# Kernel tuning notes

Hardware: AMD Instinct MI355X
Metric: run time of the kernel (lower is better)

Reference implementation:

```python
import jax, jax.numpy as jnp
import numpy as np

V, E, T, U, C, B = 50000, 300, 512, 256, 20, 64


def _rn(k, shape):
    return jax.random.normal(k, shape, jnp.float32) * 0.05


def setup_inputs() -> dict:
    key = jax.random.key(0)
    ks = jax.random.split(key, 16)
    G = 3 * U  # gate width (z, r, h)
    return {
        "x": jax.random.randint(ks[0], (B, T), 0, V),
        "emb": _rn(ks[1], (V, E)),
        "k1f": _rn(ks[2], (E, G)), "rk1f": _rn(ks[3], (U, G)), "b1f": jnp.zeros((2, G), jnp.float32),
        "k1b": _rn(ks[4], (E, G)), "rk1b": _rn(ks[5], (U, G)), "b1b": jnp.zeros((2, G), jnp.float32),
        "k2f": _rn(ks[6], (2 * U, G)), "rk2f": _rn(ks[7], (U, G)), "b2f": jnp.zeros((2, G), jnp.float32),
        "k2b": _rn(ks[8], (2 * U, G)), "rk2b": _rn(ks[9], (U, G)), "b2b": jnp.zeros((2, G), jnp.float32),
        "wout": _rn(ks[10], (2 * U, C)), "bout": jnp.zeros((C,), jnp.float32),
    }


def gru_dir(x_seq, k, rk, b, reverse):
    """Keras GRU (reset_after=True), one direction. x_seq: [B,T,D] -> [B,T,U]."""
    # precompute input projections for all timesteps (big GEMM once)
    xw = jnp.einsum('btd,dg->btg', x_seq, k) + b[0]  # [B,T,3U]
    if reverse:
        xw = xw[:, ::-1]
    u = rk.shape[0]

    def step(h, xt):
        inner = h @ rk + b[1]                      # [B,3U]
        xz, xr, xh = jnp.split(xt, 3, axis=-1)
        rz, rr, rh = jnp.split(inner, 3, axis=-1)
        z = jax.nn.sigmoid(xz + rz)
        r = jax.nn.sigmoid(xr + rr)
        hh = jnp.tanh(xh + r * rh)
        hn = z * h + (1.0 - z) * hh
        return hn, hn

    h0 = jnp.zeros((x_seq.shape[0], u), x_seq.dtype)
    _, hs = jax.lax.scan(step, h0, jnp.swapaxes(xw, 0, 1))  # [T,B,U]
    hs = jnp.swapaxes(hs, 0, 1)                             # [B,T,U]
    return hs[:, ::-1] if reverse else hs


def reference(x, emb, k1f, rk1f, b1f, k1b, rk1b, b1b,
              k2f, rk2f, b2f, k2b, rk2b, b2b, wout, bout):
    e = emb[x]                                   # [B,T,E]
    # BiGRU layer 1 (return_sequences=True), concat merge
    f1 = gru_dir(e, k1f, rk1f, b1f, reverse=False)
    b1 = gru_dir(e, k1b, rk1b, b1b, reverse=True)
    h1 = jnp.concatenate([f1, b1], axis=-1)      # [B,T,2U]
    # BiGRU layer 2 (return_sequences=False): last state of each direction
    f2 = gru_dir(h1, k2f, rk2f, b2f, reverse=False)[:, -1]  # [B,U]
    b2 = gru_dir(h1, k2b, rk2b, b2b, reverse=True)[:, 0]    # [B,U]
    h2 = jnp.concatenate([f2, b2], axis=-1)      # [B,2U]
    return jax.nn.softmax(h2 @ wout + bout, axis=-1)  # [B,C]
```

## Files before the change

### kernel.cpp

```cpp
#include <hip/hip_runtime.h>

typedef unsigned char  u8;
typedef unsigned short u16;
typedef unsigned int   u32;
typedef unsigned long long u64;
typedef __attribute__((ext_vector_type(8))) short s8v;
typedef __attribute__((ext_vector_type(4))) float f4v;
typedef __attribute__((ext_vector_type(4))) int   i4v;
typedef __attribute__((ext_vector_type(8))) int   i8v;
typedef __attribute__((ext_vector_type(2))) unsigned int u32x2;

#define B_SZ  64
#define T_LEN 512
#define U_DIM 256
#define E_DIM 300
#define EP    320
#define G3    768
#define NTOT  1536
#define C_DIM 20
#define BT    (B_SZ*T_LEN)

__device__ __forceinline__ float bf2f(u16 h){ return __uint_as_float(((u32)h)<<16); }
__device__ __forceinline__ u16 f2bf(float f){
  u32 u = __float_as_uint(f);
  u32 r = (u + 0x7FFFu + ((u>>16)&1u)) >> 16;
  return (u16)r;
}

__device__ __forceinline__ u8 f2fp8(float f){
  u32 u = __float_as_uint(f);
  u32 s = (u>>24)&0x80u;
  u32 au = u & 0x7fffffffu;
  if(au < 0x3C800000u){
    float m = rintf(__uint_as_float(au) * 512.f);
    return (u8)(s | (u32)(int)m);
  }
  int e = (int)(au>>23) - 127;
  u32 mant = au & 0x7fffffu;
  u32 lsb = (mant>>20)&1u;
  mant += 0x7FFFFu + lsb;
  if(mant >> 23){ mant = 0; e += 1; }
  if(e > 8 || (e==8 && ((mant>>20)&7u)==7u)) return (u8)(s | 0x7Eu);
  return (u8)(s | ((u32)(e+7)<<3) | ((mant>>20)&7u));
}

__global__ void embed_pad(const int* __restrict__ x, const float* __restrict__ emb,
                          u16* __restrict__ e){
  int idx = blockIdx.x*256 + threadIdx.x;
  if(idx >= BT*EP) return;
  int row = idx / EP, col = idx - row*EP;
  u16 v = 0;
  if(col < E_DIM) v = f2bf(emb[(size_t)x[row]*E_DIM + col]);
  e[idx] = v;
}

__global__ void transpose_cc(const float* __restrict__ A, const float* __restrict__ Bm,
                             u16* __restrict__ dst, int K, int Kp, int N){
  int idx = blockIdx.x*256 + threadIdx.x;
  if(idx >= N*Kp) return;
  int n = idx / Kp, k = idx - n*Kp;
  u16 v = 0;
  if(k < K){
    const float* s = (n < G3) ? A : Bm;
    int nn = (n < G3) ? n : n - G3;
    v = f2bf(s[(size_t)k*G3 + nn]);
  }
  dst[idx] = v;
}

__global__ void transpose_fp8(const float* __restrict__ rk, u8* __restrict__ dst){
  int idx = blockIdx.x*256 + threadIdx.x;
  if(idx >= G3*U_DIM) return;
  int n = idx >> 8, k = idx & 255;
  dst[idx] = f2fp8(rk[(size_t)k*G3 + n]);
}

__global__ __launch_bounds__(256) void gemm_bt(
    const u16* __restrict__ A, const u16* __restrict__ BT_, u16* __restrict__ Cq,
    int Kp, const float* __restrict__ biasA, const float* __restrict__ biasB)
{
  __shared__ u16 Al[128][40];
  __shared__ u16 Bl[128][40];
  int tid = threadIdx.x;
  int w = tid>>6, l = tid&63, lc = l&15, quad = l>>4;
  int wm = w>>1, wn = w&1;
  int nb = blockIdx.x*128;
  int bg4 = blockIdx.y >> 4, tg = blockIdx.y & 15;
  int b0r = bg4*4, tb0 = tg*32;

  f4v acc[4][4];
  #pragma unroll
  for(int i=0;i<4;i++)
    #pragma unroll
    for(int j=0;j<4;j++) acc[i][j] = (f4v){0.f,0.f,0.f,0.f};

  int nk = Kp >> 5;
  for(int kt=0; kt<nk; kt++){
    __syncthreads();
    {
      int c0 = tid, c1 = tid + 256;
      int r0 = c0>>2, k80 = c0&3;
      int r1 = c1>>2, k81 = c1&3;
      size_t ga0 = ((size_t)(b0r + (r0&3))*T_LEN + tb0 + (r0>>2))*Kp;
      size_t ga1 = ((size_t)(b0r + (r1&3))*T_LEN + tb0 + (r1>>2))*Kp;
      *(s8v*)&Al[r0][k80*8] = *(const s8v*)(A + ga0 + kt*32 + k80*8);
      *(s8v*)&Al[r1][k81*8] = *(const s8v*)(A + ga1 + kt*32 + k81*8);
      *(s8v*)&Bl[r0][k80*8] = *(const s8v*)(BT_ + (size_t)(nb+r0)*Kp + kt*32 + k80*8);
      *(s8v*)&Bl[r1][k81*8] = *(const s8v*)(BT_ + (size_t)(nb+r1)*Kp + kt*32 + k81*8);
    }
    __syncthreads();
    s8v af[4], bf[4];
    #pragma unroll
    for(int i=0;i<4;i++) af[i] = *(const s8v*)&Al[wm*64 + i*16 + lc][quad*8];
    #pragma unroll
    for(int j=0;j<4;j++) bf[j] = *(const s8v*)&Bl[wn*64 + j*16 + lc][quad*8];
    #pragma unroll
    for(int i=0;i<4;i++)
      #pragma unroll
      for(int j=0;j<4;j++)
        acc[i][j] = __builtin_amdgcn_mfma_f32_16x16x32_bf16(af[i], bf[j], acc[i][j],0,0,0);
  }

  int dirq = (nb >= G3) ? 1 : 0;
  int c7b  = nb - dirq*G3 + wn*64;
  int g    = c7b >> 8;
  int ut0  = (c7b >> 4) & 15;
  const float* bb = dirq ? biasB : biasA;
  float bj[4];
  #pragma unroll
  for(int j=0;j<4;j++){
    int cc = c7b + j*16 + lc;
    bj[j] = bb[cc] + ((g < 2) ? bb[G3 + cc] : 0.f);
  }
  #pragma unroll
  for(int i=0;i<4;i++){
    int t = tb0 + wm*16 + i*4 + quad;
    size_t base = ((((size_t)dirq*T_LEN + t)*B_SZ + b0r)*3 + g)*256 + lc*16 + ut0;
    #pragma unroll
    for(int r=0;r<4;r++){
      u16 p0 = f2bf(acc[i][0][r] + bj[0]);
      u16 p1 = f2bf(acc[i][1][r] + bj[1]);
      u16 p2 = f2bf(acc[i][2][r] + bj[2]);
      u16 p3 = f2bf(acc[i][3][r] + bj[3]);
      *(u64*)(Cq + base + (size_t)r*768) =
        (u64)p0 | ((u64)p1<<16) | ((u64)p2<<32) | ((u64)p3<<48);
    }
  }
}


#define ACLB \
 "a0","a1","a2","a3","a4","a5","a6","a7","a8","a9","a10","a11","a12","a13","a14","a15", \
 "a16","a17","a18","a19","a20","a21","a22","a23","a24","a25","a26","a27","a28","a29","a30","a31", \
 "a32","a33","a34","a35","a36","a37","a38","a39","a40","a41","a42","a43","a44","a45","a46","a47", \
 "a48","a49","a50","a51","a52","a53","a54","a55","a56","a57","a58","a59","a60","a61","a62","a63", \
 "a64","a65","a66","a67","a68","a69","a70","a71","a72","a73","a74","a75","a76","a77","a78","a79", \
 "a80","a81","a82","a83","a84","a85","a86","a87","a88","a89","a90","a91","a92","a93","a94","a95", \
 "a96","a97","a98","a99","a100","a101","a102","a103","a104","a105","a106","a107","a108","a109","a110","a111", \
 "a112","a113","a114","a115","a116","a117","a118","a119","a120","a121","a122","a123","a124","a125","a126","a127", \
 "a128","a129","a130","a131","a132","a133","a134","a135","a136","a137","a138","a139","a140","a141","a142","a143", \
 "a144","a145","a146","a147","a148","a149","a150","a151","a152","a153","a154","a155","a156","a157","a158","a159", \
 "a160","a161","a162","a163","a164","a165","a166","a167","a168","a169","a170","a171","a172","a173","a174","a175", \
 "a176","a177","a178","a179","a180","a181","a182","a183","a184","a185","a186","a187","a188","a189","a190","a191"

#define AFENCE asm volatile("" ::: ACLB)

#define BINIT8(G,S,KT,A0,A1,A2,A3,A4,A5,A6,A7) { \
  const u8* p = rkd + ((size_t)((G)*256 + w*64 + (S)*16 + lc)<<8) + (KT)*128 + quad*32; \
  i4v t0 = *(const i4v*)p; \
  i4v t1 = *(const i4v*)(p+16); \
  asm volatile("v_accvgpr_write_b32 a" #A0 ", %0\n\t" \
               "v_accvgpr_write_b32 a" #A1 ", %1\n\t" \
               "v_accvgpr_write_b32 a" #A2 ", %2\n\t" \
               "v_accvgpr_write_b32 a" #A3 ", %3\n\t" \
               "v_accvgpr_write_b32 a" #A4 ", %4\n\t" \
               "v_accvgpr_write_b32 a" #A5 ", %5\n\t" \
               "v_accvgpr_write_b32 a" #A6 ", %6\n\t" \
               "v_accvgpr_write_b32 a" #A7 ", %7" \
               :: "v"(t0[0]),"v"(t0[1]),"v"(t0[2]),"v"(t0[3]), \
                  "v"(t1[0]),"v"(t1[1]),"v"(t1[2]),"v"(t1[3]) : ACLB); }

#define MFZ8(ACC,AF,AR) \
  asm("v_mfma_f32_16x16x128_f8f6f4 %0, %1, " AR ", 0" : "=&v"(ACC) : "v"(AF))
#define MFA8(ACC,AF,AR) \
  asm("v_mfma_f32_16x16x128_f8f6f4 %0, %1, " AR ", %0" : "+v"(ACC) : "v"(AF))

#define FENCE12 asm volatile("s_nop 7\n\ts_nop 7" \
  : "+v"(acc[0]),"+v"(acc[1]),"+v"(acc[2]),"+v"(acc[3]), \
    "+v"(acc[4]),"+v"(acc[5]),"+v"(acc[6]),"+v"(acc[7]), \
    "+v"(acc[8]),"+v"(acc[9]),"+v"(acc[10]),"+v"(acc[11]) :: ACLB)

#define LBAR asm volatile("s_waitcnt lgkmcnt(0)\n\ts_barrier" ::: ACLB, "memory")

__device__ __forceinline__ float bsel(u32x2 v, int i){
  u32 wv = (i & 2) ? (u32)v[1] : (u32)v[0];
  return __uint_as_float((i & 1) ? (wv & 0xffff0000u) : (wv << 16));
}

#define GATE(UT) { \
  float xz = bsel(cz, UT); \
  float xr = bsel(cr, UT); \
  float xh = bsel(ch, UT); \
  float zf = acc[UT][0]   + xz; \
  float rf = acc[4+UT][0] + xr; \
  float rh = acc[8+UT][0] + b1h[UT]; \
  zf = __builtin_amdgcn_rcpf(1.f + __expf(-zf)); \
  rf = __builtin_amdgcn_rcpf(1.f + __expf(-rf)); \
  float hc = xh + rf*rh; \
  float e2 = __expf(2.f*hc); \
  float th = 1.f - 2.f*__builtin_amdgcn_rcpf(e2 + 1.f); \
  float hn = th + zf*(hpc[UT] - th); \
  hpc[UT] = hn; \
  u32 q8; asm("v_cvt_pk_fp8_f32 %0, %1, %2" : "=v"(q8) : "v"(hn), "v"(hn)); \
  hb8[nxt][quad*4][w*64 + (UT)*16 + lc] = (u8)(q8 & 0xffu); \
  if(MODE == 0) \
    hp[(UT)*16] = f2bf(hn); \
  else if(step == T_LEN-1) \
    h2out[(size_t)(b0+quad)*(2*U_DIM) + dir*U_DIM + w*64 + (UT)*16 + lc] = hn; \
}

template<int MODE>
__global__ __launch_bounds__(256,1) void gru_scan3(
    const u16* __restrict__ xq,
    const u8*  __restrict__ rkq,
    const float* __restrict__ bF, const float* __restrict__ bB,
    u16* __restrict__ h1out,
    float* __restrict__ h2out)
{
  int dir = blockIdx.x & 1, bg = blockIdx.x >> 1;
  int b0 = bg*4;
  int tid = threadIdx.x;
  int w = tid>>6, l = tid&63, lc = l&15, quad = l>>4;

  __shared__ u8 hb8[2][16][272];
  for(int i=tid; i<2*16*272; i+=256) ((u8*)hb8)[i] = 0;

  const u8* rkd = rkq + (size_t)dir*G3*U_DIM;

  BINIT8(0,0,0,  0,1,2,3,4,5,6,7)        BINIT8(0,0,1,  8,9,10,11,12,13,14,15)
  BINIT8(0,1,0, 16,17,18,19,20,21,22,23) BINIT8(0,1,1, 24,25,26,27,28,29,30,31)
  BINIT8(0,2,0, 32,33,34,35,36,37,38,39) BINIT8(0,2,1, 40,41,42,43,44,45,46,47)
  BINIT8(0,3,0, 48,49,50,51,52,53,54,55) BINIT8(0,3,1, 56,57,58,59,60,61,62,63)
  BINIT8(1,0,0, 64,65,66,67,68,69,70,71) BINIT8(1,0,1, 72,73,74,75,76,77,78,79)
  BINIT8(1,1,0, 80,81,82,83,84,85,86,87) BINIT8(1,1,1, 88,89,90,91,92,93,94,95)
  BINIT8(1,2,0, 96,97,98,99,100,101,102,103) BINIT8(1,2,1, 104,105,106,107,108,109,110,111)
  BINIT8(1,3,0, 112,113,114,115,116,117,118,119) BINIT8(1,3,1, 120,121,122,123,124,125,126,127)
  BINIT8(2,0,0, 128,129,130,131,132,133,134,135) BINIT8(2,0,1, 136,137,138,139,140,141,142,143)
  BINIT8(2,1,0, 144,145,146,147,148,149,150,151) BINIT8(2,1,1, 152,153,154,155,156,157,158,159)
  BINIT8(2,2,0, 160,161,162,163,164,165,166,167) BINIT8(2,2,1, 168,169,170,171,172,173,174,175)
  BINIT8(2,3,0, 176,177,178,179,180,181,182,183) BINIT8(2,3,1, 184,185,186,187,188,189,190,191)

  float b1h[4];
  const float* bias1 = (dir ? bB : bF) + G3;
  #pragma unroll
  for(int ut=0; ut<4; ut++) b1h[ut] = bias1[2*U_DIM + w*64 + ut*16 + lc];

  int t0 = dir ? (T_LEN-1) : 0;
  long qstride = dir ? -(long)(64*3*256) : (long)(64*3*256);
  const u16* xp = xq + ((((size_t)dir*T_LEN + t0)*B_SZ + (b0+quad))*3)*256 + lc*16 + w*4;
  long hstride = dir ? -(long)(2*U_DIM) : (long)(2*U_DIM);
  u16* hp = (MODE==0)
    ? (h1out + ((size_t)(b0+quad)*T_LEN + t0)*(2*U_DIM) + dir*U_DIM + w*64 + lc)
    : nullptr;

  float hpc[4] = {0.f, 0.f, 0.f, 0.f};

  u32x2 cz = *(const u32x2*)(xp);
  u32x2 cr = *(const u32x2*)(xp + 256);
  u32x2 ch = *(const u32x2*)(xp + 512);

  __syncthreads();

  int cur = 0;
  for(int step=0; step<T_LEN; step++){
    AFENCE;
    int nxt = cur ^ 1;

    i8v af0, af1;
    {
      const u8* p = &hb8[cur][lc][quad*32];
      i4v lo0 = *(const i4v*)p,        hi0 = *(const i4v*)(p+16);
      i4v lo1 = *(const i4v*)(p+128),  hi1 = *(const i4v*)(p+144);
      af0 = __builtin_shufflevector(lo0, hi0, 0,1,2,3,4,5,6,7);
      af1 = __builtin_shufflevector(lo1, hi1, 0,1,2,3,4,5,6,7);
    }

    const u16* xpn = xp + qstride;
    u32x2 czn = *(const u32x2*)(xpn);
    u32x2 crn = *(const u32x2*)(xpn + 256);
    u32x2 chn = *(const u32x2*)(xpn + 512);

    f4v acc[12];
    MFZ8(acc[0], af0,"a[0:7]");     MFZ8(acc[1], af0,"a[16:23]");
    MFZ8(acc[2], af0,"a[32:39]");   MFZ8(acc[3], af0,"a[48:55]");
    MFZ8(acc[4], af0,"a[64:71]");   MFZ8(acc[5], af0,"a[80:87]");
    MFZ8(acc[6], af0,"a[96:103]");  MFZ8(acc[7], af0,"a[112:119]");
    MFZ8(acc[8], af0,"a[128:135]"); MFZ8(acc[9], af0,"a[144:151]");
    MFZ8(acc[10],af0,"a[160:167]"); MFZ8(acc[11],af0,"a[176:183]");
    MFA8(acc[0], af1,"a[8:15]");    MFA8(acc[1], af1,"a[24:31]");
    MFA8(acc[2], af1,"a[40:47]");   MFA8(acc[3], af1,"a[56:63]");
    MFA8(acc[4], af1,"a[72:79]");   MFA8(acc[5], af1,"a[88:95]");
    MFA8(acc[6], af1,"a[104:111]"); MFA8(acc[7], af1,"a[120:127]");
    MFA8(acc[8], af1,"a[136:143]"); MFA8(acc[9], af1,"a[152:159]");
    MFA8(acc[10],af1,"a[168:175]"); MFA8(acc[11],af1,"a[184:191]");
    FENCE12;

    GATE(0)
    GATE(1)
    GATE(2)
    GATE(3)

    cz = czn; cr = crn; ch = chn;
    xp = xpn;
    if(MODE==0) hp += hstride;
    LBAR;
    cur ^= 1;
  }
}

__global__ void out_softmax(const float* __restrict__ h2, const float* __restrict__ wout,
                            const float* __restrict__ bout, float* __restrict__ out)
{
  __shared__ float lg[C_DIM];
  int b = blockIdx.x, l = threadIdx.x;
  float acc[C_DIM];
  #pragma unroll
  for(int c=0;c<C_DIM;c++) acc[c] = 0.f;
  for(int k=l; k<2*U_DIM; k+=64){
    float hv = h2[b*2*U_DIM + k];
    #pragma unroll
    for(int c=0;c<C_DIM;c++) acc[c] += hv * wout[k*C_DIM + c];
  }
  #pragma unroll
  for(int c=0;c<C_DIM;c++){
    float v = acc[c];
    for(int off=32; off; off>>=1) v += __shfl_down(v, off);
    if(l==0) lg[c] = v + bout[c];
  }
  __syncthreads();
  if(l==0){
    float mx = lg[0];
    for(int c=1;c<C_DIM;c++) mx = fmaxf(mx, lg[c]);
    float sum = 0.f, ex[C_DIM];
    for(int c=0;c<C_DIM;c++){ ex[c] = __expf(lg[c]-mx); sum += ex[c]; }
    for(int c=0;c<C_DIM;c++) out[b*C_DIM + c] = ex[c]/sum;
  }
}

extern "C" void kernel_launch(void* const* d_in, const int* in_sizes, int n_in,
                              void* d_out, int out_size, void* d_ws, size_t ws_size,
                              hipStream_t stream)
{
  const int*   x    = (const int*)d_in[0];
  const float* emb  = (const float*)d_in[1];
  const float* k1f  = (const float*)d_in[2];
  const float* rk1f = (const float*)d_in[3];
  const float* b1f  = (const float*)d_in[4];
  const float* k1b  = (const float*)d_in[5];
  const float* rk1b = (const float*)d_in[6];
  const float* b1b  = (const float*)d_in[7];
  const float* k2f  = (const float*)d_in[8];
  const float* rk2f = (const float*)d_in[9];
  const float* b2f  = (const float*)d_in[10];
  const float* k2b  = (const float*)d_in[11];
  const float* rk2b = (const float*)d_in[12];
  const float* b2b  = (const float*)d_in[13];
  const float* wout = (const float*)d_in[14];
  const float* bout = (const float*)d_in[15];

  char* ws = (char*)d_ws;
  u16*  k1t   = (u16*)(ws);
  u16*  k2t   = (u16*)(ws + 983040);
  u8*   rkq   = (u8*)(ws + 2555904);
  float* h2   = (float*)(ws + 4128768);
  u16*  h1    = (u16*)(ws + 4259840);
  u16*  e_pad = (u16*)(ws + 4259840);
  u16*  xq    = (u16*)(ws + 37814272);

  transpose_cc<<<(NTOT*EP +255)/256,256,0,stream>>>(k1f, k1b, k1t, E_DIM, EP, NTOT);
  transpose_cc<<<(NTOT*512+255)/256,256,0,stream>>>(k2f, k2b, k2t, 512, 512, NTOT);
  transpose_fp8<<<768,256,0,stream>>>(rk1f, rkq);
  transpose_fp8<<<768,256,0,stream>>>(rk1b, rkq + 1*G3*U_DIM);
  transpose_fp8<<<768,256,0,stream>>>(rk2f, rkq + 2*G3*U_DIM);
  transpose_fp8<<<768,256,0,stream>>>(rk2b, rkq + 3*G3*U_DIM);

  embed_pad<<<(BT*EP)/256,256,0,stream>>>(x, emb, e_pad);

  gemm_bt<<<dim3(12,256),256,0,stream>>>(e_pad, k1t, xq, EP, b1f, b1b);
  gru_scan3<0><<<32,256,0,stream>>>(xq, rkq, b1f, b1b, h1, nullptr);

  gemm_bt<<<dim3(12,256),256,0,stream>>>(h1, k2t, xq, 512, b2f, b2b);
  gru_scan3<1><<<32,256,0,stream>>>(xq, rkq + 2*G3*U_DIM, b2f, b2b, nullptr, h2);

  out_softmax<<<64,64,0,stream>>>(h2, wout, bout, (float*)d_out);
}
```

Baseline: 1.119 ms.

## Split GRU recurrence across eight waves and interleave MFMA groups with gates

The recurrent scan kernel now launches 512 threads per block instead of 256. Each wave owns 32 hidden units instead of 64, so it keeps half as many recurrent weight tiles in AGPRs and issues 12 MFMAs per step instead of 24. The MFMAs are split into two groups of three gates each, wrapped in s_setprio, so the gate math for the first half-tile can overlap with the second group's MFMAs. The aim is to shorten the serial per-timestep latency chain, at the cost of a barrier across twice as many waves.

Result: slower. 1.237 ms (+10.5%).

```diff
diff --git a/kernel.cpp b/kernel.cpp
--- a/kernel.cpp
+++ b/kernel.cpp
@@ -8,7 +8,6 @@
 typedef __attribute__((ext_vector_type(4))) float f4v;
 typedef __attribute__((ext_vector_type(4))) int   i4v;
 typedef __attribute__((ext_vector_type(8))) int   i8v;
-typedef __attribute__((ext_vector_type(2))) unsigned int u32x2;
 
 #define B_SZ  64
 #define T_LEN 512
@@ -155,18 +154,12 @@
  "a32","a33","a34","a35","a36","a37","a38","a39","a40","a41","a42","a43","a44","a45","a46","a47", \
  "a48","a49","a50","a51","a52","a53","a54","a55","a56","a57","a58","a59","a60","a61","a62","a63", \
  "a64","a65","a66","a67","a68","a69","a70","a71","a72","a73","a74","a75","a76","a77","a78","a79", \
- "a80","a81","a82","a83","a84","a85","a86","a87","a88","a89","a90","a91","a92","a93","a94","a95", \
- "a96","a97","a98","a99","a100","a101","a102","a103","a104","a105","a106","a107","a108","a109","a110","a111", \
- "a112","a113","a114","a115","a116","a117","a118","a119","a120","a121","a122","a123","a124","a125","a126","a127", \
- "a128","a129","a130","a131","a132","a133","a134","a135","a136","a137","a138","a139","a140","a141","a142","a143", \
- "a144","a145","a146","a147","a148","a149","a150","a151","a152","a153","a154","a155","a156","a157","a158","a159", \
- "a160","a161","a162","a163","a164","a165","a166","a167","a168","a169","a170","a171","a172","a173","a174","a175", \
- "a176","a177","a178","a179","a180","a181","a182","a183","a184","a185","a186","a187","a188","a189","a190","a191"
+ "a80","a81","a82","a83","a84","a85","a86","a87","a88","a89","a90","a91","a92","a93","a94","a95"
 
 #define AFENCE asm volatile("" ::: ACLB)
 
 #define BINIT8(G,S,KT,A0,A1,A2,A3,A4,A5,A6,A7) { \
-  const u8* p = rkd + ((size_t)((G)*256 + w*64 + (S)*16 + lc)<<8) + (KT)*128 + quad*32; \
+  const u8* p = rkd + ((size_t)((G)*256 + w*32 + (S)*16 + lc)<<8) + (KT)*128 + quad*32; \
   i4v t0 = *(const i4v*)p; \
   i4v t1 = *(const i4v*)(p+16); \
   asm volatile("v_accvgpr_write_b32 a" #A0 ", %0\n\t" \
@@ -185,25 +178,24 @@
 #define MFA8(ACC,AF,AR) \
   asm("v_mfma_f32_16x16x128_f8f6f4 %0, %1, " AR ", %0" : "+v"(ACC) : "v"(AF))
 
-#define FENCE12 asm volatile("s_nop 7\n\ts_nop 7" \
-  : "+v"(acc[0]),"+v"(acc[1]),"+v"(acc[2]),"+v"(acc[3]), \
-    "+v"(acc[4]),"+v"(acc[5]),"+v"(acc[6]),"+v"(acc[7]), \
-    "+v"(acc[8]),"+v"(acc[9]),"+v"(acc[10]),"+v"(acc[11]) :: ACLB)
+#define FENCEA asm volatile("s_nop 7\n\ts_nop 7" \
+  : "+v"(acc[0]),"+v"(acc[2]),"+v"(acc[4]) :: ACLB)
+#define FENCEB asm volatile("s_nop 7\n\ts_nop 7" \
+  : "+v"(acc[1]),"+v"(acc[3]),"+v"(acc[5]) :: ACLB)
 
 #define LBAR asm volatile("s_waitcnt lgkmcnt(0)\n\ts_barrier" ::: ACLB, "memory")
 
-__device__ __forceinline__ float bsel(u32x2 v, int i){
-  u32 wv = (i & 2) ? (u32)v[1] : (u32)v[0];
-  return __uint_as_float((i & 1) ? (wv & 0xffff0000u) : (wv << 16));
+__device__ __forceinline__ float bsel2(u32 v, int i){
+  return __uint_as_float(i ? (v & 0xffff0000u) : (v << 16));
 }
 
 #define GATE(UT) { \
-  float xz = bsel(cz, UT); \
-  float xr = bsel(cr, UT); \
-  float xh = bsel(ch, UT); \
+  float xz = bsel2(cz, UT); \
+  float xr = bsel2(cr, UT); \
+  float xh = bsel2(ch, UT); \
   float zf = acc[UT][0]   + xz; \
-  float rf = acc[4+UT][0] + xr; \
-  float rh = acc[8+UT][0] + b1h[UT]; \
+  float rf = acc[2+UT][0] + xr; \
+  float rh = acc[4+UT][0] + b1h[UT]; \
   zf = __builtin_amdgcn_rcpf(1.f + __expf(-zf)); \
   rf = __builtin_amdgcn_rcpf(1.f + __expf(-rf)); \
   float hc = xh + rf*rh; \
@@ -212,15 +204,15 @@
   float hn = th + zf*(hpc[UT] - th); \
   hpc[UT] = hn; \
   u32 q8; asm("v_cvt_pk_fp8_f32 %0, %1, %2" : "=v"(q8) : "v"(hn), "v"(hn)); \
-  hb8[nxt][quad*4][w*64 + (UT)*16 + lc] = (u8)(q8 & 0xffu); \
+  hb8[nxt][quad*4][w*32 + (UT)*16 + lc] = (u8)(q8 & 0xffu); \
   if(MODE == 0) \
     hp[(UT)*16] = f2bf(hn); \
   else if(step == T_LEN-1) \
-    h2out[(size_t)(b0+quad)*(2*U_DIM) + dir*U_DIM + w*64 + (UT)*16 + lc] = hn; \
+    h2out[(size_t)(b0+quad)*(2*U_DIM) + dir*U_DIM + w*32 + (UT)*16 + lc] = hn; \
 }
 
 template<int MODE>
-__global__ __launch_bounds__(256,1) void gru_scan3(
+__global__ __launch_bounds__(512,2) void gru_scan3(
     const u16* __restrict__ xq,
     const u8*  __restrict__ rkq,
     const float* __restrict__ bF, const float* __restrict__ bB,
@@ -233,41 +225,35 @@
   int w = tid>>6, l = tid&63, lc = l&15, quad = l>>4;
 
   __shared__ u8 hb8[2][16][272];
-  for(int i=tid; i<2*16*272; i+=256) ((u8*)hb8)[i] = 0;
+  for(int i=tid; i<2*16*272; i+=512) ((u8*)hb8)[i] = 0;
 
   const u8* rkd = rkq + (size_t)dir*G3*U_DIM;
 
   BINIT8(0,0,0,  0,1,2,3,4,5,6,7)        BINIT8(0,0,1,  8,9,10,11,12,13,14,15)
   BINIT8(0,1,0, 16,17,18,19,20,21,22,23) BINIT8(0,1,1, 24,25,26,27,28,29,30,31)
-  BINIT8(0,2,0, 32,33,34,35,36,37,38,39) BINIT8(0,2,1, 40,41,42,43,44,45,46,47)
-  BINIT8(0,3,0, 48,49,50,51,52,53,54,55) BINIT8(0,3,1, 56,57,58,59,60,61,62,63)
-  BINIT8(1,0,0, 64,65,66,67,68,69,70,71) BINIT8(1,0,1, 72,73,74,75,76,77,78,79)
-  BINIT8(1,1,0, 80,81,82,83,84,85,86,87) BINIT8(1,1,1, 88,89,90,91,92,93,94,95)
-  BINIT8(1,2,0, 96,97,98,99,100,101,102,103) BINIT8(1,2,1, 104,105,106,107,108,109,110,111)
-  BINIT8(1,3,0, 112,113,114,115,116,117,118,119) BINIT8(1,3,1, 120,121,122,123,124,125,126,127)
-  BINIT8(2,0,0, 128,129,130,131,132,133,134,135) BINIT8(2,0,1, 136,137,138,139,140,141,142,143)
-  BINIT8(2,1,0, 144,145,146,147,148,149,150,151) BINIT8(2,1,1, 152,153,154,155,156,157,158,159)
-  BINIT8(2,2,0, 160,161,162,163,164,165,166,167) BINIT8(2,2,1, 168,169,170,171,172,173,174,175)
-  BINIT8(2,3,0, 176,177,178,179,180,181,182,183) BINIT8(2,3,1, 184,185,186,187,188,189,190,191)
-
-  float b1h[4];
+  BINIT8(1,0,0, 32,33,34,35,36,37,38,39) BINIT8(1,0,1, 40,41,42,43,44,45,46,47)
+  BINIT8(1,1,0, 48,49,50,51,52,53,54,55) BINIT8(1,1,1, 56,57,58,59,60,61,62,63)
+  BINIT8(2,0,0, 64,65,66,67,68,69,70,71) BINIT8(2,0,1, 72,73,74,75,76,77,78,79)
+  BINIT8(2,1,0, 80,81,82,83,84,85,86,87) BINIT8(2,1,1, 88,89,90,91,92,93,94,95)
+
+  float b1h[2];
   const float* bias1 = (dir ? bB : bF) + G3;
   #pragma unroll
-  for(int ut=0; ut<4; ut++) b1h[ut] = bias1[2*U_DIM + w*64 + ut*16 + lc];
+  for(int ut=0; ut<2; ut++) b1h[ut] = bias1[2*U_DIM + w*32 + ut*16 + lc];
 
   int t0 = dir ? (T_LEN-1) : 0;
   long qstride = dir ? -(long)(64*3*256) : (long)(64*3*256);
-  const u16* xp = xq + ((((size_t)dir*T_LEN + t0)*B_SZ + (b0+quad))*3)*256 + lc*16 + w*4;
+  const u16* xp = xq + ((((size_t)dir*T_LEN + t0)*B_SZ + (b0+quad))*3)*256 + lc*16 + w*2;
   long hstride = dir ? -(long)(2*U_DIM) : (long)(2*U_DIM);
   u16* hp = (MODE==0)
-    ? (h1out + ((size_t)(b0+quad)*T_LEN + t0)*(2*U_DIM) + dir*U_DIM + w*64 + lc)
+    ? (h1out + ((size_t)(b0+quad)*T_LEN + t0)*(2*U_DIM) + dir*U_DIM + w*32 + lc)
     : nullptr;
 
-  float hpc[4] = {0.f, 0.f, 0.f, 0.f};
-
-  u32x2 cz = *(const u32x2*)(xp);
-  u32x2 cr = *(const u32x2*)(xp + 256);
-  u32x2 ch = *(const u32x2*)(xp + 512);
+  float hpc[2] = {0.f, 0.f};
+
+  u32 cz = *(const u32*)(xp);
+  u32 cr = *(const u32*)(xp + 256);
+  u32 ch = *(const u32*)(xp + 512);
 
   __syncthreads();
 
@@ -286,29 +272,33 @@
     }
 
     const u16* xpn = xp + qstride;
-    u32x2 czn = *(const u32x2*)(xpn);
-    u32x2 crn = *(const u32x2*)(xpn + 256);
-    u32x2 chn = *(const u32x2*)(xpn + 512);
-
-    f4v acc[12];
-    MFZ8(acc[0], af0,"a[0:7]");     MFZ8(acc[1], af0,"a[16:23]");
-    MFZ8(acc[2], af0,"a[32:39]");   MFZ8(acc[3], af0,"a[48:55]");
-    MFZ8(acc[4], af0,"a[64:71]");   MFZ8(acc[5], af0,"a[80:87]");
-    MFZ8(acc[6], af0,"a[96:103]");  MFZ8(acc[7], af0,"a[112:119]");
-    MFZ8(acc[8], af0,"a[128:135]"); MFZ8(acc[9], af0,"a[144:151]");
-    MFZ8(acc[10],af0,"a[160:167]"); MFZ8(acc[11],af0,"a[176:183]");
-    MFA8(acc[0], af1,"a[8:15]");    MFA8(acc[1], af1,"a[24:31]");
-    MFA8(acc[2], af1,"a[40:47]");   MFA8(acc[3], af1,"a[56:63]");
-    MFA8(acc[4], af1,"a[72:79]");   MFA8(acc[5], af1,"a[88:95]");
-    MFA8(acc[6], af1,"a[104:111]"); MFA8(acc[7], af1,"a[120:127]");
-    MFA8(acc[8], af1,"a[136:143]"); MFA8(acc[9], af1,"a[152:159]");
-    MFA8(acc[10],af1,"a[168:175]"); MFA8(acc[11],af1,"a[184:191]");
-    FENCE12;
-
+    u32 czn = *(const u32*)(xpn);
+    u32 crn = *(const u32*)(xpn + 256);
+    u32 chn = *(const u32*)(xpn + 512);
+
+    f4v acc[6];
+
+    __builtin_amdgcn_s_setprio(1);
+    MFZ8(acc[0], af0,"a[0:7]");
+    MFZ8(acc[2], af0,"a[32:39]");
+    MFZ8(acc[4], af0,"a[64:71]");
+    MFA8(acc[0], af1,"a[8:15]");
+    MFA8(acc[2], af1,"a[40:47]");
+    MFA8(acc[4], af1,"a[72:79]");
+    __builtin_amdgcn_s_setprio(0);
+    FENCEA;
     GATE(0)
+
+    __builtin_amdgcn_s_setprio(1);
+    MFZ8(acc[1], af0,"a[16:23]");
+    MFZ8(acc[3], af0,"a[48:55]");
+    MFZ8(acc[5], af0,"a[80:87]");
+    MFA8(acc[1], af1,"a[24:31]");
+    MFA8(acc[3], af1,"a[56:63]");
+    MFA8(acc[5], af1,"a[88:95]");
+    __builtin_amdgcn_s_setprio(0);
+    FENCEB;
     GATE(1)
-    GATE(2)
-    GATE(3)
 
     cz = czn; cr = crn; ch = chn;
     xp = xpn;
@@ -387,10 +377,10 @@
   embed_pad<<<(BT*EP)/256,256,0,stream>>>(x, emb, e_pad);
 
   gemm_bt<<<dim3(12,256),256,0,stream>>>(e_pad, k1t, xq, EP, b1f, b1b);
-  gru_scan3<0><<<32,256,0,stream>>>(xq, rkq, b1f, b1b, h1, nullptr);
+  gru_scan3<0><<<32,512,0,stream>>>(xq, rkq, b1f, b1b, h1, nullptr);
 
   gemm_bt<<<dim3(12,256),256,0,stream>>>(h1, k2t, xq, 512, b2f, b2b);
-  gru_scan3<1><<<32,256,0,stream>>>(xq, rkq + 2*G3*U_DIM, b2f, b2b, nullptr, h2);
+  gru_scan3<1><<<32,512,0,stream>>>(xq, rkq + 2*G3*U_DIM, b2f, b2b, nullptr, h2);
 
   out_softmax<<<64,64,0,stream>>>(h2, wout, bout, (float*)d_out);
 }
```
